# Kernel tuning notes

Hardware: AMD Instinct MI355X
Metric: run time of the kernel (lower is better)

## Reference

```python
import jax, jax.numpy as jnp
import numpy as np

N_HEADS = 12

def setup_inputs() -> dict:
    key = jax.random.key(0)
    k1, k2, k3 = jax.random.split(key, 3)
    B, S, W = 8, 1024, 768
    x = jax.random.normal(k1, (B, S, W), dtype=jnp.float32)
    w_qkv = jax.random.normal(k2, (W, 3 * W), dtype=jnp.float32) * (W ** -0.5)
    w_out = jax.random.normal(k3, (W, W), dtype=jnp.float32) * (W ** -0.5)
    return {"x": x, "w_qkv": w_qkv, "w_out": w_out}

def reference(x, w_qkv, w_out):
    B, S, W = x.shape
    H = N_HEADS
    D = W // H  # head_width
    scale = W ** -0.5  # NOTE: source scales by width**-0.5, not head_width**-0.5
    qkv = x @ w_qkv  # [B, S, 3W]
    q, k, v = jnp.split(qkv, 3, axis=2)
    q = q.reshape(B, S, H, D)
    k = k.reshape(B, S, H, D)
    # attn_score: [B, i, j, n]
    attn_score = jnp.einsum('binh,bjnh->bijn', q, k) * scale
    attn_weight = jax.nn.softmax(attn_score, axis=2)
    # NOTE: source uses K (not V) here — faithful reproduction of the bug.
    out = jnp.einsum('bijn,bjnh->binh', attn_weight, k)
    out = out.reshape(B, S, W)
    return out @ w_out  # dropout is identity in eval
```

## Files before the change

kernel.cpp:

```cpp
#include <hip/hip_runtime.h>

#define US unsigned short

typedef __bf16 bf16x8 __attribute__((ext_vector_type(8)));
typedef short s16x8 __attribute__((ext_vector_type(8)));
typedef short s16x4 __attribute__((ext_vector_type(4)));
typedef float f32x4 __attribute__((ext_vector_type(4)));

static __device__ __forceinline__ US f2bf(float f) {
  union { float f; unsigned u; } x; x.f = f;
  unsigned r = x.u + 0x7fffu + ((x.u >> 16) & 1u);
  return (US)(r >> 16);
}

static __device__ __forceinline__ unsigned cvtpk(float lo, float hi) {
  unsigned r;
  asm("v_cvt_pk_bf16_f32 %0, %1, %2" : "=v"(r) : "v"(lo), "v"(hi));
  return r;
}

static __device__ __forceinline__ void gload16(const US* g, US* l) {
  __builtin_amdgcn_global_load_lds(
      (const __attribute__((address_space(1))) void*)g,
      (__attribute__((address_space(3))) void*)l, 16, 0, 0);
}

__global__ __launch_bounds__(256) void prep(
    const float* __restrict__ x, const float* __restrict__ wqkv,
    const float* __restrict__ wout, US* __restrict__ xb,
    US* __restrict__ wqkT, US* __restrict__ woutT, float cexp) {
  __shared__ float t[32][33];
  const int bid = blockIdx.x, tid = threadIdx.x;
  if (bid < 3072) {
    int i = bid * 256 + tid;
    const float4* s = (const float4*)x + (size_t)i * 2;
    float4 a = s[0], b = s[1];
    s16x8 w;
    w[0] = (short)f2bf(a.x); w[1] = (short)f2bf(a.y);
    w[2] = (short)f2bf(a.z); w[3] = (short)f2bf(a.w);
    w[4] = (short)f2bf(b.x); w[5] = (short)f2bf(b.y);
    w[6] = (short)f2bf(b.z); w[7] = (short)f2bf(b.w);
    *(s16x8*)(xb + (size_t)i * 8) = w;
    return;
  }
  const float* src;
  US* dst;
  int n0, r0, C, nlim;
  float scale;
  if (bid < 4224) {
    int tb = bid - 3072;
    n0 = (tb % 48) * 32; r0 = (tb / 48) * 32;
    src = wqkv; dst = wqkT; C = 2304; nlim = 768; scale = cexp;
  } else {
    int tb = bid - 4224;
    n0 = (tb % 24) * 32; r0 = (tb / 24) * 32;
    src = wout; dst = woutT; C = 768; nlim = 0; scale = 1.0f;
  }
  const int R = 768;
  int tx = tid & 31, ty = tid >> 5;
  for (int i = 0; i < 4; ++i) {
    int r = i * 8 + ty;
    t[r][tx] = src[(size_t)(r0 + r) * C + n0 + tx];
  }
  __syncthreads();
  for (int i = 0; i < 4; ++i) {
    int n = i * 8 + ty;
    float s = (n0 + n < nlim) ? scale : 1.0f;
    dst[(size_t)(n0 + n) * R + r0 + tx] = f2bf(t[tx][n] * s);
  }
}

__global__ __launch_bounds__(256) void kt_transpose(
    const US* __restrict__ QK, US* __restrict__ KT) {
  __shared__ US t[32][34];
  int bh = blockIdx.z, b = bh / 12, h = bh % 12;
  int s0 = blockIdx.x * 32, d0 = blockIdx.y * 32;
  int tx = threadIdx.x & 31, ty = threadIdx.x >> 5;
  const US* src = QK + ((size_t)b * 1024 + s0) * 1536 + 768 + h * 64 + d0;
  for (int i = 0; i < 4; ++i)
    t[i * 8 + ty][tx] = src[(size_t)(i * 8 + ty) * 1536 + tx];
  __syncthreads();
  US* dst = KT + ((size_t)bh * 64 + d0) * 1024 + s0;
  for (int i = 0; i < 4; ++i)
    dst[(size_t)(i * 8 + ty) * 1024 + tx] = t[tx][i * 8 + ty];
}

template<int OUT_BF16, int FUSE_KT>
__global__ __launch_bounds__(256) void gemm_bt(
    const US* __restrict__ A, const US* __restrict__ Bt,
    void* __restrict__ Cv, int M, int N, int K, US* __restrict__ KT) {
  __shared__ US As[2][128 * 32];
  __shared__ US Bs[2][128 * 32];
  const int tid = threadIdx.x;
  const int wave = tid >> 6, lane = tid & 63;
  const int lr = lane & 15, lg = lane >> 4;
  const int m0 = blockIdx.x * 128, n0 = blockIdx.y * 128;
  const int wr = (wave >> 1) * 64, wc = (wave & 1) * 64;
  const int srow = tid >> 2;
  const int sseg = (tid & 3) ^ (srow & 3);
  const US* gA = A + (size_t)(m0 + srow) * K + sseg * 8;
  const US* gB = Bt + (size_t)(n0 + srow) * K + sseg * 8;

  f32x4 acc[4][4];
  for (int i = 0; i < 4; ++i)
    for (int j = 0; j < 4; ++j) acc[i][j] = (f32x4){0.f, 0.f, 0.f, 0.f};

  const int nIt = K >> 5;
  for (int i = 0; i < 2; ++i) {
    gload16(gA + (size_t)i * 64 * K, &As[0][tid * 8 + i * 2048]);
    gload16(gB + (size_t)i * 64 * K, &Bs[0][tid * 8 + i * 2048]);
  }
  __syncthreads();

  for (int it = 0; it < nIt; ++it) {
    if (it + 1 < nIt) {
      int k0 = (it + 1) * 32, bb = (it + 1) & 1;
      for (int i = 0; i < 2; ++i) {
        gload16(gA + (size_t)i * 64 * K + k0, &As[bb][tid * 8 + i * 2048]);
        gload16(gB + (size_t)i * 64 * K + k0, &Bs[bb][tid * 8 + i * 2048]);
      }
    }
    const US* Ab = As[it & 1];
    const US* Bb = Bs[it & 1];
    bf16x8 af[4], bfr[4];
    for (int mi = 0; mi < 4; ++mi)
      af[mi] = *(const bf16x8*)(Ab + (wr + mi * 16 + lr) * 32 + ((lg ^ (lr & 3)) * 8));
    for (int ni = 0; ni < 4; ++ni)
      bfr[ni] = *(const bf16x8*)(Bb + (wc + ni * 16 + lr) * 32 + ((lg ^ (lr & 3)) * 8));
    for (int mi = 0; mi < 4; ++mi)
      for (int ni = 0; ni < 4; ++ni)
        acc[mi][ni] = __builtin_amdgcn_mfma_f32_16x16x32_bf16(
            af[mi], bfr[ni], acc[mi][ni], 0, 0, 0);
    __syncthreads();
  }

  for (int mi = 0; mi < 4; ++mi)
    for (int ni = 0; ni < 4; ++ni)
      for (int r = 0; r < 4; ++r) {
        size_t row = (size_t)m0 + wr + mi * 16 + lg * 4 + r;
        size_t col = (size_t)n0 + wc + ni * 16 + lr;
        float v = acc[mi][ni][r];
        if (OUT_BF16) ((US*)Cv)[row * N + col] = f2bf(v);
        else          ((float*)Cv)[row * N + col] = v;
      }

  if (FUSE_KT && n0 >= 768) {
    const int h = (n0 + wc - 768) >> 6;
    const int bb = m0 >> 10;
    const int sb = (m0 & 1023) + wr + lg * 4;
    US* ktp = KT + (size_t)(bb * 12 + h) * 64 * 1024;
    for (int mi = 0; mi < 4; ++mi)
      for (int ni = 0; ni < 4; ++ni) {
        int d = ni * 16 + lr;
        s16x4 w;
        w[0] = (short)f2bf(acc[mi][ni][0]);
        w[1] = (short)f2bf(acc[mi][ni][1]);
        w[2] = (short)f2bf(acc[mi][ni][2]);
        w[3] = (short)f2bf(acc[mi][ni][3]);
        *(s16x4*)(ktp + (size_t)d * 1024 + sb + mi * 16) = w;
      }
  }
}

static __device__ __forceinline__ void softmax_route(
    const f32x4 sv[4], float& lsum, bool odd, bool hi, int laneQ0, int laneQ1,
    bf16x8& pa0v, bf16x8& pa1v) {
  float p[4][4];
#pragma unroll
  for (int ns = 0; ns < 4; ++ns)
#pragma unroll
    for (int r = 0; r < 4; ++r) {
      p[ns][r] = __builtin_amdgcn_exp2f(sv[ns][r]);
      lsum += p[ns][r];
    }
  unsigned pk00 = cvtpk(p[0][0], p[0][1]), pk01 = cvtpk(p[0][2], p[0][3]);
  unsigned pk10 = cvtpk(p[1][0], p[1][1]), pk11 = cvtpk(p[1][2], p[1][3]);
  unsigned pk20 = cvtpk(p[2][0], p[2][1]), pk21 = cvtpk(p[2][2], p[2][3]);
  unsigned pk30 = cvtpk(p[3][0], p[3][1]), pk31 = cvtpk(p[3][2], p[3][3]);
  int a0 = (int)(odd ? pk10 : pk00), a1 = (int)(odd ? pk11 : pk01);
  int a2 = (int)(odd ? pk30 : pk20), a3 = (int)(odd ? pk31 : pk21);
  int b0 = (int)(odd ? pk00 : pk10), b1 = (int)(odd ? pk01 : pk11);
  int b2 = (int)(odd ? pk20 : pk30), b3 = (int)(odd ? pk21 : pk31);
  int r0 = __shfl(a0, laneQ0), r1 = __shfl(a1, laneQ0);
  int r2 = __shfl(a2, laneQ0), r3 = __shfl(a3, laneQ0);
  int r4 = __shfl(b0, laneQ1), r5 = __shfl(b1, laneQ1);
  int r6 = __shfl(b2, laneQ1), r7 = __shfl(b3, laneQ1);
  union { unsigned u[4]; bf16x8 v; } pa0, pa1;
  pa0.u[0] = hi ? (unsigned)r4 : (unsigned)r0;
  pa0.u[1] = hi ? (unsigned)r5 : (unsigned)r1;
  pa0.u[2] = hi ? (unsigned)r0 : (unsigned)r4;
  pa0.u[3] = hi ? (unsigned)r1 : (unsigned)r5;
  pa1.u[0] = hi ? (unsigned)r6 : (unsigned)r2;
  pa1.u[1] = hi ? (unsigned)r7 : (unsigned)r3;
  pa1.u[2] = hi ? (unsigned)r2 : (unsigned)r6;
  pa1.u[3] = hi ? (unsigned)r3 : (unsigned)r7;
  pa0v = pa0.v;
  pa1v = pa1.v;
}

__global__ __launch_bounds__(256, 3) void attn_kernel(
    const US* __restrict__ QK, const US* __restrict__ KTg, US* __restrict__ AO) {
  __shared__ US Kr[2][64 * 64];
  __shared__ US Kt[2][64 * 64];
  const int tid = threadIdx.x, wave = tid >> 6, lane = tid & 63;
  const int lr = lane & 15, lg = lane >> 4;
  const int id = blockIdx.y * 8 + blockIdx.x;
  const int bh = (id & 7) * 12 + ((id >> 3) % 12);
  const int qt = id / 96;
  const int b = bh / 12, h = bh % 12;
  const int qw = qt * 128 + wave * 32;
  const size_t rowbase = (size_t)b * 1024;
  const US* Qp = QK + rowbase * 1536 + h * 64;
  const US* Kp = QK + rowbase * 1536 + 768 + h * 64;
  const US* KTp = KTg + (size_t)bh * 64 * 1024;

  const int srow = tid >> 3;
  const int sseg = (tid & 7) ^ (srow & 7);
  const US* gK = Kp + (size_t)srow * 1536 + sseg * 8;
  const US* gT = KTp + (size_t)srow * 1024 + sseg * 8;

  bf16x8 qf0[2], qf1[2];
#pragma unroll
  for (int kk = 0; kk < 2; ++kk) {
    qf0[kk] = *(const bf16x8*)(Qp + (size_t)(qw + lr) * 1536 + kk * 32 + lg * 8);
    qf1[kk] = *(const bf16x8*)(Qp + (size_t)(qw + 16 + lr) * 1536 + kk * 32 + lg * 8);
  }

  const bool odd = (lg & 1) != 0;
  const bool hi = (lg >> 1) != 0;
  const int laneQ0 = lr + 32 * (lg & 1) + 16 * (lg >> 1);
  const int laneQ1 = lr + 32 * (lg & 1) + 16 * (1 - (lg >> 1));

  float lsum0 = 0.f, lsum1 = 0.f;
  f32x4 acc0[4], acc1[4];
#pragma unroll
  for (int d = 0; d < 4; ++d) {
    acc0[d] = (f32x4){0.f, 0.f, 0.f, 0.f};
    acc1[d] = (f32x4){0.f, 0.f, 0.f, 0.f};
  }

  for (int i = 0; i < 2; ++i) {
    gload16(gK + (size_t)(i * 32) * 1536, &Kr[0][tid * 8 + i * 2048]);
    gload16(gT + (size_t)(i * 32) * 1024, &Kt[0][tid * 8 + i * 2048]);
  }
  __syncthreads();

  for (int t = 0; t < 16; ++t) {
    if (t + 1 < 16) {
      int kv0 = (t + 1) * 64, bb = (t + 1) & 1;
      for (int i = 0; i < 2; ++i) {
        gload16(gK + (size_t)(kv0 + i * 32) * 1536, &Kr[bb][tid * 8 + i * 2048]);
        gload16(gT + (size_t)(i * 32) * 1024 + kv0, &Kt[bb][tid * 8 + i * 2048]);
      }
    }
    const US* Krb = Kr[t & 1];
    const US* Ktb = Kt[t & 1];

    f32x4 sv0[4], sv1[4];
    __builtin_amdgcn_s_setprio(1);
#pragma unroll
    for (int ns = 0; ns < 4; ++ns) {
      f32x4 a0 = {0.f, 0.f, 0.f, 0.f}, a1 = {0.f, 0.f, 0.f, 0.f};
#pragma unroll
      for (int kk = 0; kk < 2; ++kk) {
        bf16x8 kf = *(const bf16x8*)(
            Krb + (ns * 16 + lr) * 64 + (((kk * 4 + lg) ^ (lr & 7)) * 8));
        a0 = __builtin_amdgcn_mfma_f32_16x16x32_bf16(kf, qf0[kk], a0, 0, 0, 0);
        a1 = __builtin_amdgcn_mfma_f32_16x16x32_bf16(kf, qf1[kk], a1, 0, 0, 0);
      }
      sv0[ns] = a0; sv1[ns] = a1;
    }
    __builtin_amdgcn_s_setprio(0);

    bf16x8 pa00, pa01, pa10, pa11;
    softmax_route(sv0, lsum0, odd, hi, laneQ0, laneQ1, pa00, pa01);
    softmax_route(sv1, lsum1, odd, hi, laneQ0, laneQ1, pa10, pa11);

    __builtin_amdgcn_s_setprio(1);
#pragma unroll
    for (int d = 0; d < 4; ++d) {
      int drow = d * 16 + lr;
      bf16x8 kf0 = *(const bf16x8*)(Ktb + drow * 64 + ((lg ^ (lr & 7)) * 8));
      bf16x8 kf1 = *(const bf16x8*)(Ktb + drow * 64 + (((4 + lg) ^ (lr & 7)) * 8));
      acc0[d] = __builtin_amdgcn_mfma_f32_16x16x32_bf16(pa00, kf0, acc0[d], 0, 0, 0);
      acc0[d] = __builtin_amdgcn_mfma_f32_16x16x32_bf16(pa01, kf1, acc0[d], 0, 0, 0);
      acc1[d] = __builtin_amdgcn_mfma_f32_16x16x32_bf16(pa10, kf0, acc1[d], 0, 0, 0);
      acc1[d] = __builtin_amdgcn_mfma_f32_16x16x32_bf16(pa11, kf1, acc1[d], 0, 0, 0);
    }
    __builtin_amdgcn_s_setprio(0);
    __syncthreads();
  }

  lsum0 += __shfl_xor(lsum0, 16);
  lsum0 += __shfl_xor(lsum0, 32);
  lsum1 += __shfl_xor(lsum1, 16);
  lsum1 += __shfl_xor(lsum1, 32);
  float inv0[4], inv1[4];
#pragma unroll
  for (int r = 0; r < 4; ++r) {
    inv0[r] = 1.0f / __shfl(lsum0, lg * 4 + r);
    inv1[r] = 1.0f / __shfl(lsum1, lg * 4 + r);
  }
#pragma unroll
  for (int d = 0; d < 4; ++d)
#pragma unroll
    for (int r = 0; r < 4; ++r) {
      size_t row0 = rowbase + qw + lg * 4 + r;
      AO[row0 * 768 + h * 64 + d * 16 + lr] = f2bf(acc0[d][r] * inv0[r]);
      size_t row1 = rowbase + qw + 16 + lg * 4 + r;
      AO[row1 * 768 + h * 64 + d * 16 + lr] = f2bf(acc1[d][r] * inv1[r]);
    }
}

extern "C" void kernel_launch(void* const* d_in, const int* in_sizes, int n_in,
                              void* d_out, int out_size, void* d_ws, size_t ws_size,
                              hipStream_t stream) {
  const float* x    = (const float*)d_in[0];
  const float* wqkv = (const float*)d_in[1];
  const float* wout = (const float*)d_in[2];
  float* out = (float*)d_out;

  US* wqkT  = (US*)d_ws;
  US* woutT = wqkT + (size_t)1536 * 768;
  US* QK    = woutT + (size_t)768 * 768;
  US* AO    = QK + (size_t)8192 * 1536;
  US* xb    = AO + (size_t)8192 * 768;
  const size_t needElems = (size_t)1536 * 768 + (size_t)768 * 768 +
                           (size_t)8192 * 1536 + (size_t)8192 * 768 * 2 +
                           (size_t)96 * 64 * 1024;
  const bool fuse = ws_size >= needElems * sizeof(US);
  US* KT = fuse ? (xb + (size_t)8192 * 768) : xb;

  const float cexp = 0.03608439182435161f * 1.4426950408889634f;

  prep<<<4800, 256, 0, stream>>>(x, wqkv, wout, xb, wqkT, woutT, cexp);
  if (fuse) {
    gemm_bt<1, 1><<<dim3(64, 12), 256, 0, stream>>>(xb, wqkT, QK, 8192, 1536, 768, KT);
  } else {
    gemm_bt<1, 0><<<dim3(64, 12), 256, 0, stream>>>(xb, wqkT, QK, 8192, 1536, 768, nullptr);
    kt_transpose<<<dim3(32, 2, 96), 256, 0, stream>>>(QK, KT);
  }
  attn_kernel<<<dim3(8, 96), 256, 0, stream>>>(QK, KT, AO);
  gemm_bt<0, 0><<<dim3(64, 6), 256, 0, stream>>>(AO, woutT, out, 8192, 768, 768, nullptr);
}
```

Measured before the change: 99.79 us.

## Read K tiles directly from global memory in attention; use smaller-tile output GEMM

The attention kernel no longer stages K and K-transpose tiles through double-buffered LDS. Each wave now loads its MFMA operands straight from global memory (through the cache), which drops the LDS footprint, the per-tile barrier and the occupancy hint. The output projection moves to a new GEMM with 64x128 tiles, launching twice as many blocks so the grid covers the CUs better. In exchange, every wave issues redundant global loads for data it used to share through LDS, and the K rows are read with a 1536-element stride, so latency may become exposed.

```diff
diff --git a/kernel.cpp b/kernel.cpp
--- a/kernel.cpp
+++ b/kernel.cpp
@@ -85,10 +85,10 @@
     dst[(size_t)(i * 8 + ty) * 1024 + tx] = t[tx][i * 8 + ty];
 }
 
-template<int OUT_BF16, int FUSE_KT>
+template<int FUSE_KT>
 __global__ __launch_bounds__(256) void gemm_bt(
     const US* __restrict__ A, const US* __restrict__ Bt,
-    void* __restrict__ Cv, int M, int N, int K, US* __restrict__ KT) {
+    US* __restrict__ Cv, int M, int N, int K, US* __restrict__ KT) {
   __shared__ US As[2][128 * 32];
   __shared__ US Bs[2][128 * 32];
   const int tid = threadIdx.x;
@@ -139,9 +139,7 @@
       for (int r = 0; r < 4; ++r) {
         size_t row = (size_t)m0 + wr + mi * 16 + lg * 4 + r;
         size_t col = (size_t)n0 + wc + ni * 16 + lr;
-        float v = acc[mi][ni][r];
-        if (OUT_BF16) ((US*)Cv)[row * N + col] = f2bf(v);
-        else          ((float*)Cv)[row * N + col] = v;
+        Cv[row * N + col] = f2bf(acc[mi][ni][r]);
       }
 
   if (FUSE_KT && n0 >= 768) {
@@ -160,6 +158,61 @@
         *(s16x4*)(ktp + (size_t)d * 1024 + sb + mi * 16) = w;
       }
   }
+}
+
+__global__ __launch_bounds__(256) void gemm_bt2(
+    const US* __restrict__ A, const US* __restrict__ Bt,
+    float* __restrict__ Cv, int M, int N, int K) {
+  __shared__ US As[2][64 * 32];
+  __shared__ US Bs[2][128 * 32];
+  const int tid = threadIdx.x;
+  const int wave = tid >> 6, lane = tid & 63;
+  const int lr = lane & 15, lg = lane >> 4;
+  const int m0 = blockIdx.x * 64, n0 = blockIdx.y * 128;
+  const int wr = (wave >> 1) * 32, wc = (wave & 1) * 64;
+  const int srow = tid >> 2;
+  const int sseg = (tid & 3) ^ (srow & 3);
+  const US* gA = A + (size_t)(m0 + srow) * K + sseg * 8;
+  const US* gB = Bt + (size_t)(n0 + srow) * K + sseg * 8;
+
+  f32x4 acc[2][4];
+  for (int i = 0; i < 2; ++i)
+    for (int j = 0; j < 4; ++j) acc[i][j] = (f32x4){0.f, 0.f, 0.f, 0.f};
+
+  const int nIt = K >> 5;
+  gload16(gA, &As[0][tid * 8]);
+  for (int i = 0; i < 2; ++i)
+    gload16(gB + (size_t)i * 64 * K, &Bs[0][tid * 8 + i * 2048]);
+  __syncthreads();
+
+  for (int it = 0; it < nIt; ++it) {
+    if (it + 1 < nIt) {
+      int k0 = (it + 1) * 32, bb = (it + 1) & 1;
+      gload16(gA + k0, &As[bb][tid * 8]);
+      for (int i = 0; i < 2; ++i)
+        gload16(gB + (size_t)i * 64 * K + k0, &Bs[bb][tid * 8 + i * 2048]);
+    }
+    const US* Ab = As[it & 1];
+    const US* Bb = Bs[it & 1];
+    bf16x8 af[2], bfr[4];
+    for (int mi = 0; mi < 2; ++mi)
+      af[mi] = *(const bf16x8*)(Ab + (wr + mi * 16 + lr) * 32 + ((lg ^ (lr & 3)) * 8));
+    for (int ni = 0; ni < 4; ++ni)
+      bfr[ni] = *(const bf16x8*)(Bb + (wc + ni * 16 + lr) * 32 + ((lg ^ (lr & 3)) * 8));
+    for (int mi = 0; mi < 2; ++mi)
+      for (int ni = 0; ni < 4; ++ni)
+        acc[mi][ni] = __builtin_amdgcn_mfma_f32_16x16x32_bf16(
+            af[mi], bfr[ni], acc[mi][ni], 0, 0, 0);
+    __syncthreads();
+  }
+
+  for (int mi = 0; mi < 2; ++mi)
+    for (int ni = 0; ni < 4; ++ni)
+      for (int r = 0; r < 4; ++r) {
+        size_t row = (size_t)m0 + wr + mi * 16 + lg * 4 + r;
+        size_t col = (size_t)n0 + wc + ni * 16 + lr;
+        Cv[row * N + col] = acc[mi][ni][r];
+      }
 }
 
 static __device__ __forceinline__ void softmax_route(
@@ -198,10 +251,8 @@
   pa1v = pa1.v;
 }
 
-__global__ __launch_bounds__(256, 3) void attn_kernel(
+__global__ __launch_bounds__(256) void attn_kernel(
     const US* __restrict__ QK, const US* __restrict__ KTg, US* __restrict__ AO) {
-  __shared__ US Kr[2][64 * 64];
-  __shared__ US Kt[2][64 * 64];
   const int tid = threadIdx.x, wave = tid >> 6, lane = tid & 63;
   const int lr = lane & 15, lg = lane >> 4;
   const int id = blockIdx.y * 8 + blockIdx.x;
@@ -214,11 +265,6 @@
   const US* Kp = QK + rowbase * 1536 + 768 + h * 64;
   const US* KTp = KTg + (size_t)bh * 64 * 1024;
 
-  const int srow = tid >> 3;
-  const int sseg = (tid & 7) ^ (srow & 7);
-  const US* gK = Kp + (size_t)srow * 1536 + sseg * 8;
-  const US* gT = KTp + (size_t)srow * 1024 + sseg * 8;
-
   bf16x8 qf0[2], qf1[2];
 #pragma unroll
   for (int kk = 0; kk < 2; ++kk) {
@@ -239,22 +285,9 @@
     acc1[d] = (f32x4){0.f, 0.f, 0.f, 0.f};
   }
 
-  for (int i = 0; i < 2; ++i) {
-    gload16(gK + (size_t)(i * 32) * 1536, &Kr[0][tid * 8 + i * 2048]);
-    gload16(gT + (size_t)(i * 32) * 1024, &Kt[0][tid * 8 + i * 2048]);
-  }
-  __syncthreads();
-
   for (int t = 0; t < 16; ++t) {
-    if (t + 1 < 16) {
-      int kv0 = (t + 1) * 64, bb = (t + 1) & 1;
-      for (int i = 0; i < 2; ++i) {
-        gload16(gK + (size_t)(kv0 + i * 32) * 1536, &Kr[bb][tid * 8 + i * 2048]);
-        gload16(gT + (size_t)(i * 32) * 1024 + kv0, &Kt[bb][tid * 8 + i * 2048]);
-      }
-    }
-    const US* Krb = Kr[t & 1];
-    const US* Ktb = Kt[t & 1];
+    const US* Kpt = Kp + (size_t)(t * 64) * 1536;
+    const US* Ktt = KTp + t * 64;
 
     f32x4 sv0[4], sv1[4];
     __builtin_amdgcn_s_setprio(1);
@@ -264,7 +297,7 @@
 #pragma unroll
       for (int kk = 0; kk < 2; ++kk) {
         bf16x8 kf = *(const bf16x8*)(
-            Krb + (ns * 16 + lr) * 64 + (((kk * 4 + lg) ^ (lr & 7)) * 8));
+            Kpt + (size_t)(ns * 16 + lr) * 1536 + kk * 32 + lg * 8);
         a0 = __builtin_amdgcn_mfma_f32_16x16x32_bf16(kf, qf0[kk], a0, 0, 0, 0);
         a1 = __builtin_amdgcn_mfma_f32_16x16x32_bf16(kf, qf1[kk], a1, 0, 0, 0);
       }
@@ -280,15 +313,14 @@
 #pragma unroll
     for (int d = 0; d < 4; ++d) {
       int drow = d * 16 + lr;
-      bf16x8 kf0 = *(const bf16x8*)(Ktb + drow * 64 + ((lg ^ (lr & 7)) * 8));
-      bf16x8 kf1 = *(const bf16x8*)(Ktb + drow * 64 + (((4 + lg) ^ (lr & 7)) * 8));
+      bf16x8 kf0 = *(const bf16x8*)(Ktt + (size_t)drow * 1024 + lg * 8);
+      bf16x8 kf1 = *(const bf16x8*)(Ktt + (size_t)drow * 1024 + 32 + lg * 8);
       acc0[d] = __builtin_amdgcn_mfma_f32_16x16x32_bf16(pa00, kf0, acc0[d], 0, 0, 0);
       acc0[d] = __builtin_amdgcn_mfma_f32_16x16x32_bf16(pa01, kf1, acc0[d], 0, 0, 0);
       acc1[d] = __builtin_amdgcn_mfma_f32_16x16x32_bf16(pa10, kf0, acc1[d], 0, 0, 0);
       acc1[d] = __builtin_amdgcn_mfma_f32_16x16x32_bf16(pa11, kf1, acc1[d], 0, 0, 0);
     }
     __builtin_amdgcn_s_setprio(0);
-    __syncthreads();
   }
 
   lsum0 += __shfl_xor(lsum0, 16);
@@ -335,11 +367,11 @@
 
   prep<<<4800, 256, 0, stream>>>(x, wqkv, wout, xb, wqkT, woutT, cexp);
   if (fuse) {
-    gemm_bt<1, 1><<<dim3(64, 12), 256, 0, stream>>>(xb, wqkT, QK, 8192, 1536, 768, KT);
+    gemm_bt<1><<<dim3(64, 12), 256, 0, stream>>>(xb, wqkT, QK, 8192, 1536, 768, KT);
   } else {
-    gemm_bt<1, 0><<<dim3(64, 12), 256, 0, stream>>>(xb, wqkT, QK, 8192, 1536, 768, nullptr);
+    gemm_bt<0><<<dim3(64, 12), 256, 0, stream>>>(xb, wqkT, QK, 8192, 1536, 768, nullptr);
     kt_transpose<<<dim3(32, 2, 96), 256, 0, stream>>>(QK, KT);
   }
   attn_kernel<<<dim3(8, 96), 256, 0, stream>>>(QK, KT, AO);
-  gemm_bt<0, 0><<<dim3(64, 6), 256, 0, stream>>>(AO, woutT, out, 8192, 768, 768, nullptr);
-}
+  gemm_bt2<<<dim3(128, 6), 256, 0, stream>>>(AO, woutT, out, 8192, 768, 768);
+}
```

After: 150.7 us. +51.1%, slower.
